# Kernel tuning notes

Measured on AMD Instinct MI355X. Metric: run time of the kernel, lower is better.

## Reference

```python
import jax, jax.numpy as jnp
import numpy as np

HIDDEN = 768
NUM_BLOCKS = 8
BLOCK = HIDDEN // NUM_BLOCKS
LAMBDA = 0.01
SCALE = 0.02


def softshrink(v, lam):
    return jnp.sign(v) * jnp.maximum(jnp.abs(v) - lam, 0.0)


def setup_inputs() -> dict:
    key = jax.random.key(0)
    ks = jax.random.split(key, 5)
    B, S = 4, 8192
    x = jax.random.normal(ks[0], (B, S, HIDDEN), dtype=jnp.float32)
    w1 = SCALE * jax.random.normal(ks[1], (2, NUM_BLOCKS, BLOCK, BLOCK), dtype=jnp.float32)
    b1 = SCALE * jax.random.normal(ks[2], (2, NUM_BLOCKS, BLOCK), dtype=jnp.float32)
    w2 = SCALE * jax.random.normal(ks[3], (2, NUM_BLOCKS, BLOCK, BLOCK), dtype=jnp.float32)
    b2 = SCALE * jax.random.normal(ks[4], (2, NUM_BLOCKS, BLOCK), dtype=jnp.float32)
    return {"x": x, "w1": w1, "b1": b1, "w2": w2, "b2": b2}


def reference(x, w1, b1, w2, b2):
    bias = x
    dtype = x.dtype
    xf = x.astype(jnp.float32)
    B, S, C = xf.shape
    M = S // 2 + 1  # total modes; hard_thresholding_fraction=1.0 -> all kept
    X = jnp.fft.rfft(xf, axis=1, norm="ortho")  # [B, M, C] complex64
    X = X.reshape(B, M, NUM_BLOCKS, BLOCK)
    xr, xi = X.real, X.imag
    # layer 1: complex block-diagonal matmul + relu
    mul = lambda inp, w: jnp.einsum("bmnd,ndk->bmnk", inp, w)
    o1r = jax.nn.relu(mul(xr, w1[0]) - mul(xi, w1[1]) + b1[0])
    o1i = jax.nn.relu(mul(xi, w1[0]) + mul(xr, w1[1]) + b1[1])
    # layer 2
    o2r = mul(o1r, w2[0]) - mul(o1i, w2[1]) + b2[0]
    o2i = mul(o1r, w2[1]) + mul(o1i, w2[0]) + b2[1]
    # softshrink applied elementwise to real and imag parts
    o2r = softshrink(o2r, LAMBDA)
    o2i = softshrink(o2i, LAMBDA)
    Y = (o2r + 1j * o2i).reshape(B, M, C)
    y = jnp.fft.irfft(Y, n=S, axis=1, norm="ortho").astype(dtype)
    return y + bias
```

## Files before the change

kernel.cpp:

```cpp
#include <hip/hip_runtime.h>
#include <hip/hip_bf16.h>

#define HIDDEN 768
#define NB 8
#define BLK 96
#define S_LEN 8192
#define H_LEN 4096
#define M_LEN 4097
#define MP 4160
#define BATCH 4
#define KBIG 192
#define TMOD 64
#define APITCH 100

#define TWO_PI 6.28318530717958647692f
#define INV_SQRT_N 0.011048543456039806f
#define C_INV 0.022097086912079612f
#define LAM 0.01f

typedef __attribute__((ext_vector_type(8))) short short8;
typedef __attribute__((ext_vector_type(4))) float float4v;

__device__ __forceinline__ short f2bf(float f) {
    __hip_bfloat16 h = __float2bfloat16(f);
    return *reinterpret_cast<short*>(&h);
}
__device__ __forceinline__ float bf2f(unsigned short s) {
    __hip_bfloat16 h = *reinterpret_cast<__hip_bfloat16*>(&s);
    return __bfloat162float(h);
}
__device__ __forceinline__ unsigned pack2bf(float a, float b) {
    return (unsigned)(unsigned short)f2bf(a) | ((unsigned)(unsigned short)f2bf(b) << 16);
}
__device__ __forceinline__ float2 cmul(float2 a, float2 b) {
    return make_float2(a.x * b.x - a.y * b.y, a.x * b.y + a.y * b.x);
}

__global__ __launch_bounds__(256) void prep_weights(const float* __restrict__ w1,
                                                    const float* __restrict__ w2,
                                                    const float* __restrict__ b1,
                                                    const float* __restrict__ b2,
                                                    short* __restrict__ WT1,
                                                    short* __restrict__ WT2,
                                                    float* __restrict__ bb1,
                                                    float* __restrict__ bb2) {
    int idx = blockIdx.x * 256 + threadIdx.x;
    if (idx < NB * KBIG * KBIG) {
        int n = idx / (KBIG * KBIG);
        int r = idx % (KBIG * KBIG);
        int op = r / KBIG;
        int kin = r % KBIG;
        int oc = op >> 1;
        int oim = op & 1;
        int d = kin >> 1;
        int im = kin & 1;
        {
            float w0 = w1[((size_t)(0 * NB + n) * BLK + d) * BLK + oc];
            float wi = w1[((size_t)(1 * NB + n) * BLK + d) * BLK + oc];
            float v = oim ? (im ? w0 : wi) : (im ? -wi : w0);
            WT1[idx] = f2bf(v);
        }
        {
            float w0 = w2[((size_t)(0 * NB + n) * BLK + d) * BLK + oc];
            float wi = w2[((size_t)(1 * NB + n) * BLK + d) * BLK + oc];
            float v = oim ? (im ? w0 : wi) : (im ? -wi : w0);
            WT2[idx] = f2bf(v);
        }
    }
    if (idx < NB * KBIG) {
        int n = idx / KBIG, op = idx % KBIG;
        int oc = op >> 1, oim = op & 1;
        bb1[idx] = oim ? b1[(1 * NB + n) * BLK + oc] : b1[(0 * NB + n) * BLK + oc];
        bb2[idx] = oim ? b2[(1 * NB + n) * BLK + oc] : b2[(0 * NB + n) * BLK + oc];
    }
}

__global__ __launch_bounds__(256) void init_twiddles(float2* __restrict__ tw4k,
                                                     float2* __restrict__ tw8k) {
    int i = blockIdx.x * 256 + threadIdx.x;
    if (i < 4096) {
        float ang = -TWO_PI * (float)i * (1.0f / 4096.0f);
        tw4k[i] = make_float2(cosf(ang), sinf(ang));
    }
    if (i <= 4096) {
        float ang = -TWO_PI * (float)i * (1.0f / 8192.0f);
        tw8k[i] = make_float2(cosf(ang), sinf(ang));
    }
}

__global__ __launch_bounds__(256) void transpose_in(const float* __restrict__ x,
                                                    __hip_bfloat16* __restrict__ xT) {
    __shared__ float t[32][33];
    const int cb = blockIdx.x, sb = blockIdx.y, b = blockIdx.z;
    const int tx = threadIdx.x & 31, ty = threadIdx.x >> 5;
    const float* xp = x + ((size_t)b * S_LEN + sb * 32) * HIDDEN + cb * 32;
    for (int i = 0; i < 4; i++)
        t[ty + 8 * i][tx] = xp[(size_t)(ty + 8 * i) * HIDDEN + tx];
    __syncthreads();
    __hip_bfloat16* xq = xT + ((size_t)b * HIDDEN + cb * 32) * S_LEN + sb * 32;
    for (int i = 0; i < 4; i++)
        xq[(size_t)(ty + 8 * i) * S_LEN + tx] = __float2bfloat16(t[tx][ty + 8 * i]);
}

template<bool INV>
__device__ __forceinline__ void dft16(float2* v) {
    const float s3 = INV ? -1.f : 1.f;
    constexpr float C1 = 0.92387953251128674f;
    constexpr float S1 = 0.38268343236508977f;
    constexpr float R2 = 0.70710678118654752f;
    float2 a[16];
    #pragma unroll
    for (int na = 0; na < 4; na++) {
        float2 x0 = v[na], x1 = v[na + 4], x2 = v[na + 8], x3 = v[na + 12];
        float t0x = x0.x + x2.x, t0y = x0.y + x2.y;
        float t1x = x0.x - x2.x, t1y = x0.y - x2.y;
        float t2x = x1.x + x3.x, t2y = x1.y + x3.y;
        float t3x = x1.x - x3.x, t3y = x1.y - x3.y;
        a[na]      = make_float2(t0x + t2x, t0y + t2y);
        a[na + 8]  = make_float2(t0x - t2x, t0y - t2y);
        a[na + 4]  = make_float2(t1x + s3 * t3y, t1y - s3 * t3x);
        a[na + 12] = make_float2(t1x - s3 * t3y, t1y + s3 * t3x);
    }
    auto tw = [s3](float2 z, float ce, float se) {
        return make_float2(z.x * ce + s3 * z.y * se, z.y * ce - s3 * z.x * se);
    };
    a[5]  = tw(a[5],  C1,  S1);
    a[6]  = tw(a[6],  R2,  R2);
    a[7]  = tw(a[7],  S1,  C1);
    a[9]  = tw(a[9],  R2,  R2);
    a[10] = tw(a[10], 0.f, 1.f);
    a[11] = tw(a[11], -R2, R2);
    a[13] = tw(a[13], S1,  C1);
    a[14] = tw(a[14], -R2, R2);
    a[15] = tw(a[15], -C1, -S1);
    #pragma unroll
    for (int kb = 0; kb < 4; kb++) {
        float2 x0 = a[4 * kb], x1 = a[4 * kb + 1], x2 = a[4 * kb + 2], x3 = a[4 * kb + 3];
        float t0x = x0.x + x2.x, t0y = x0.y + x2.y;
        float t1x = x0.x - x2.x, t1y = x0.y - x2.y;
        float t2x = x1.x + x3.x, t2y = x1.y + x3.y;
        float t3x = x1.x - x3.x, t3y = x1.y - x3.y;
        v[kb]      = make_float2(t0x + t2x, t0y + t2y);
        v[kb + 8]  = make_float2(t0x - t2x, t0y - t2y);
        v[kb + 4]  = make_float2(t1x + s3 * t3y, t1y - s3 * t3x);
        v[kb + 12] = make_float2(t1x - s3 * t3y, t1y + s3 * t3x);
    }
}

template<bool INV>
__device__ __forceinline__ void fft3pass(float2* v, float2* arr,
                                         const float2* __restrict__ tw4k, int t) {
    const float sg = INV ? -1.f : 1.f;
    const int n0 = t & 15;
    const int hi = t >> 4;

    dft16<INV>(v);
    arr[n0 * 17 + hi] = v[0];
    #pragma unroll
    for (int p = 1; p < 16; p++) {
        float2 w = tw4k[(t * p) & 4095];
        arr[(n0 + 16 * p) * 17 + hi] = cmul(v[p], make_float2(w.x, sg * w.y));
    }
    __syncthreads();

    #pragma unroll
    for (int n1 = 0; n1 < 16; n1++) v[n1] = arr[t * 17 + n1];
    __syncthreads();
    dft16<INV>(v);
    arr[hi * 17 + n0] = v[0];
    #pragma unroll
    for (int q = 1; q < 16; q++) {
        float2 w = tw4k[(16 * n0 * q) & 4095];
        arr[(hi + 16 * q) * 17 + n0] = cmul(v[q], make_float2(w.x, sg * w.y));
    }
    __syncthreads();

    #pragma unroll
    for (int i = 0; i < 16; i++) v[i] = arr[t * 17 + i];
    dft16<INV>(v);
}

__global__ __launch_bounds__(256, 4) void fft_fwd(const __hip_bfloat16* __restrict__ xT,
                                                  unsigned int* __restrict__ Xc,
                                                  const float2* __restrict__ tw4k,
                                                  const float2* __restrict__ tw8k) {
    __shared__ __align__(16) float2 arr[256 * 17];
    const int wg = blockIdx.x;
    const int t = threadIdx.x;
    const __hip_bfloat162* xrow = (const __hip_bfloat162*)(xT + (size_t)wg * S_LEN);

    float2 v[16];
    #pragma unroll
    for (int j = 0; j < 16; j++) {
        __hip_bfloat162 pz = xrow[t + 256 * j];
        v[j] = make_float2(__bfloat162float(pz.x), __bfloat162float(pz.y));
    }

    fft3pass<false>(v, arr, tw4k, t);

    __syncthreads();
    #pragma unroll
    for (int k0 = 0; k0 < 16; k0++) arr[t + 256 * k0] = v[k0];
    __syncthreads();

    unsigned int* Xrow = Xc + (size_t)wg * MP;
    for (int m = t; m <= H_LEN; m += 256) {
        int ia = m & (H_LEN - 1);
        int ib = (H_LEN - m) & (H_LEN - 1);
        float2 za = arr[ia];
        float2 zb = arr[ib];
        float er = 0.5f * (za.x + zb.x), ei = 0.5f * (za.y - zb.y);
        float dr = za.x - zb.x, di = za.y + zb.y;
        float or_ = 0.5f * di, oi = -0.5f * dr;
        float2 tt = tw8k[m];
        float xrv = (er + tt.x * or_ - tt.y * oi) * INV_SQRT_N;
        float xiv = (ei + tt.x * oi + tt.y * or_) * INV_SQRT_N;
        unsigned wd = (unsigned short)f2bf(xrv) | ((unsigned)(unsigned short)f2bf(xiv) << 16);
        Xrow[m] = wd;
    }
}

__global__ __launch_bounds__(256, 3) void mlp_mfma(const short* __restrict__ WT1,
                                                   const short* __restrict__ WT2,
                                                   const float* __restrict__ bb1,
                                                   const float* __restrict__ bb2,
                                                   unsigned int* __restrict__ Xc) {
    __shared__ __align__(16) unsigned int actA[TMOD * APITCH];
    __shared__ __align__(16) unsigned int actB[TMOD * APITCH];
    const int tid = threadIdx.x;
    const int chunk = blockIdx.x;
    const int n = blockIdx.y;
    const int b = blockIdx.z;
    const int m0 = chunk * TMOD;
    unsigned int* __restrict__ Xrow0 =
        Xc + ((size_t)b * HIDDEN + (size_t)n * BLK) * MP + m0;

    const int w = tid >> 6;
    const int l15 = tid & 15;
    const int q = (tid >> 4) & 3;
    const int outw = w * 48;
    const int mstg = tid & 63;

    #pragma unroll
    for (int dp = 0; dp < 6; dp++) {
        int d0 = dp * 16 + w * 4;
        uint4 vv;
        vv.x = Xrow0[(size_t)(d0 + 0) * MP + mstg];
        vv.y = Xrow0[(size_t)(d0 + 1) * MP + mstg];
        vv.z = Xrow0[(size_t)(d0 + 2) * MP + mstg];
        vv.w = Xrow0[(size_t)(d0 + 3) * MP + mstg];
        *(uint4*)&actA[mstg * APITCH + d0] = vv;
    }

    short8 wf[3][6];
    for (int nl = 0; nl < 3; nl++)
        for (int ks = 0; ks < 6; ks++)
            wf[nl][ks] = *(const short8*)(WT1 + ((size_t)n * KBIG + outw + nl * 16 + l15) * KBIG + ks * 32 + q * 8);

    __syncthreads();

    for (int mt = 0; mt < 4; mt++) {
        float4v acc[3];
        for (int nl = 0; nl < 3; nl++)
            acc[nl] = *(const float4v*)(bb1 + n * KBIG + outw + nl * 16 + q * 4);
        #pragma unroll
        for (int ks = 0; ks < 6; ks++) {
            short8 bf = *(const short8*)(&actA[(mt * 16 + l15) * APITCH + ks * 16 + q * 4]);
            acc[0] = __builtin_amdgcn_mfma_f32_16x16x32_bf16(wf[0][ks], bf, acc[0], 0, 0, 0);
            acc[1] = __builtin_amdgcn_mfma_f32_16x16x32_bf16(wf[1][ks], bf, acc[1], 0, 0, 0);
            acc[2] = __builtin_amdgcn_mfma_f32_16x16x32_bf16(wf[2][ks], bf, acc[2], 0, 0, 0);
        }
        #pragma unroll
        for (int nl = 0; nl < 3; nl++) {
            uint2 st;
            st.x = pack2bf(fmaxf(acc[nl][0], 0.f), fmaxf(acc[nl][1], 0.f));
            st.y = pack2bf(fmaxf(acc[nl][2], 0.f), fmaxf(acc[nl][3], 0.f));
            *(uint2*)&actB[(mt * 16 + l15) * APITCH + outw / 2 + nl * 8 + q * 2] = st;
        }
    }

    short8 wf2[3][6];
    for (int nl = 0; nl < 3; nl++)
        for (int ks = 0; ks < 6; ks++)
            wf2[nl][ks] = *(const short8*)(WT2 + ((size_t)n * KBIG + outw + nl * 16 + l15) * KBIG + ks * 32 + q * 8);

    __syncthreads();

    for (int mt = 0; mt < 4; mt++) {
        float4v acc[3];
        for (int nl = 0; nl < 3; nl++)
            acc[nl] = *(const float4v*)(bb2 + n * KBIG + outw + nl * 16 + q * 4);
        #pragma unroll
        for (int ks = 0; ks < 6; ks++) {
            short8 bf = *(const short8*)(&actB[(mt * 16 + l15) * APITCH + ks * 16 + q * 4]);
            acc[0] = __builtin_amdgcn_mfma_f32_16x16x32_bf16(wf2[0][ks], bf, acc[0], 0, 0, 0);
            acc[1] = __builtin_amdgcn_mfma_f32_16x16x32_bf16(wf2[1][ks], bf, acc[1], 0, 0, 0);
            acc[2] = __builtin_amdgcn_mfma_f32_16x16x32_bf16(wf2[2][ks], bf, acc[2], 0, 0, 0);
        }
        #pragma unroll
        for (int nl = 0; nl < 3; nl++) {
            float v0 = acc[nl][0], v1 = acc[nl][1], v2 = acc[nl][2], v3 = acc[nl][3];
            v0 = copysignf(fmaxf(fabsf(v0) - LAM, 0.f), v0);
            v1 = copysignf(fmaxf(fabsf(v1) - LAM, 0.f), v1);
            v2 = copysignf(fmaxf(fabsf(v2) - LAM, 0.f), v2);
            v3 = copysignf(fmaxf(fabsf(v3) - LAM, 0.f), v3);
            uint2 st;
            st.x = pack2bf(v0, v1);
            st.y = pack2bf(v2, v3);
            *(uint2*)&actA[(mt * 16 + l15) * APITCH + outw / 2 + nl * 8 + q * 2] = st;
        }
    }
    __syncthreads();

    #pragma unroll
    for (int dp = 0; dp < 6; dp++) {
        int d0 = dp * 16 + w * 4;
        uint4 vv = *(const uint4*)&actA[mstg * APITCH + d0];
        Xrow0[(size_t)(d0 + 0) * MP + mstg] = vv.x;
        Xrow0[(size_t)(d0 + 1) * MP + mstg] = vv.y;
        Xrow0[(size_t)(d0 + 2) * MP + mstg] = vv.z;
        Xrow0[(size_t)(d0 + 3) * MP + mstg] = vv.w;
    }
}

__global__ __launch_bounds__(256, 4) void fft_inv(const unsigned int* __restrict__ Xc,
                                                  __hip_bfloat16* __restrict__ yT,
                                                  const float2* __restrict__ tw4k,
                                                  const float2* __restrict__ tw8k) {
    __shared__ __align__(16) float2 arr[256 * 17];
    const int wg = blockIdx.x;
    const int t = threadIdx.x;
    const unsigned int* Xrow = Xc + (size_t)wg * MP;

    float2 v[16];
    #pragma unroll
    for (int j = 0; j < 16; j++) {
        int m = t + 256 * j;
        unsigned va = Xrow[m];
        unsigned vb = Xrow[H_LEN - m];
        float arv = bf2f((unsigned short)(va & 0xFFFF));
        float aiv = bf2f((unsigned short)(va >> 16));
        float brv = bf2f((unsigned short)(vb & 0xFFFF));
        float biv = bf2f((unsigned short)(vb >> 16));
        if (m == 0) { aiv = 0.f; biv = 0.f; }
        float er = 0.5f * (arv + brv), ei = 0.5f * (aiv - biv);
        float dr = arv - brv, di = aiv + biv;
        float2 tt = tw8k[m];
        float wcs = tt.x, wsn = -tt.y;
        float or_ = 0.5f * (wcs * dr - wsn * di);
        float oi = 0.5f * (wcs * di + wsn * dr);
        v[j] = make_float2(er - oi, ei + or_);
    }

    fft3pass<true>(v, arr, tw4k, t);

    __hip_bfloat162* orow = (__hip_bfloat162*)(yT + (size_t)wg * S_LEN);
    #pragma unroll
    for (int k0 = 0; k0 < 16; k0++) {
        __hip_bfloat162 w;
        w.x = __float2bfloat16(C_INV * v[k0].x);
        w.y = __float2bfloat16(C_INV * v[k0].y);
        orow[t + 256 * k0] = w;
    }
}

__global__ __launch_bounds__(256) void add_out(const __hip_bfloat16* __restrict__ yT,
                                               const float* __restrict__ x,
                                               float* __restrict__ out) {
    __shared__ float t[32][33];
    const int cb = blockIdx.x, sb = blockIdx.y, b = blockIdx.z;
    const int tx = threadIdx.x & 31, ty = threadIdx.x >> 5;
    const __hip_bfloat16* yp = yT + ((size_t)b * HIDDEN + cb * 32) * S_LEN + sb * 32;
    for (int i = 0; i < 4; i++)
        t[ty + 8 * i][tx] = __bfloat162float(yp[(size_t)(ty + 8 * i) * S_LEN + tx]);
    __syncthreads();
    const size_t off = ((size_t)b * S_LEN + sb * 32) * HIDDEN + cb * 32;
    const float* xp = x + off;
    float* op = out + off;
    for (int i = 0; i < 4; i++)
        op[(size_t)(ty + 8 * i) * HIDDEN + tx] =
            xp[(size_t)(ty + 8 * i) * HIDDEN + tx] + t[tx][ty + 8 * i];
}

extern "C" void kernel_launch(void* const* d_in, const int* in_sizes, int n_in,
                              void* d_out, int out_size, void* d_ws, size_t ws_size,
                              hipStream_t stream) {
    const float* x  = (const float*)d_in[0];
    const float* w1 = (const float*)d_in[1];
    const float* b1 = (const float*)d_in[2];
    const float* w2 = (const float*)d_in[3];
    const float* b2 = (const float*)d_in[4];
    float* out = (float*)d_out;

    char* p = (char*)d_ws;
    __hip_bfloat16* xT = (__hip_bfloat16*)p;           p += (size_t)BATCH * HIDDEN * S_LEN * 2;
    unsigned int*   Xc = (unsigned int*)p;             p += (size_t)BATCH * HIDDEN * MP * 4;
    short* WT1 = (short*)p;                            p += (size_t)NB * KBIG * KBIG * 2;
    short* WT2 = (short*)p;                            p += (size_t)NB * KBIG * KBIG * 2;
    float* bb1 = (float*)p;                            p += (size_t)NB * KBIG * 4;
    float* bb2 = (float*)p;                            p += (size_t)NB * KBIG * 4;
    float2* tw4k = (float2*)p;                         p += (size_t)4096 * sizeof(float2);
    float2* tw8k = (float2*)p;                         p += (size_t)4100 * sizeof(float2);

    prep_weights<<<(NB * KBIG * KBIG + 255) / 256, 256, 0, stream>>>(
        w1, w2, b1, b2, WT1, WT2, bb1, bb2);

    init_twiddles<<<17, 256, 0, stream>>>(tw4k, tw8k);

    transpose_in<<<dim3(HIDDEN / 32, S_LEN / 32, BATCH), 256, 0, stream>>>(x, xT);

    fft_fwd<<<BATCH * HIDDEN, 256, 0, stream>>>(xT, Xc, tw4k, tw8k);

    mlp_mfma<<<dim3(65, NB, BATCH), 256, 0, stream>>>(WT1, WT2, bb1, bb2, Xc);

    fft_inv<<<BATCH * HIDDEN, 256, 0, stream>>>(Xc, xT , tw4k, tw8k);

    add_out<<<dim3(HIDDEN / 32, S_LEN / 32, BATCH), 256, 0, stream>>>(xT, x, out);
}
```

Baseline: 387.7 us.

## Vectorize transposes with 64x64 tiles and halve MLP mode tile size

The input and output transposes now use 64x64 tiles, with float4 and short4 global accesses in place of scalar ones, to cut global memory transactions. The MLP kernel processes 32 modes per block instead of 64, which doubles the grid (129 chunks) for better occupancy and load balance. In exchange, each MLP block reloads its weight fragments for half as much work, and the larger LDS tiles in the transposes may reduce occupancy there.

```diff
diff --git a/kernel.cpp b/kernel.cpp
--- a/kernel.cpp
+++ b/kernel.cpp
@@ -10,7 +10,7 @@
 #define MP 4160
 #define BATCH 4
 #define KBIG 192
-#define TMOD 64
+#define TMOD 32
 #define APITCH 100
 
 #define TWO_PI 6.28318530717958647692f
@@ -90,16 +90,35 @@
 
 __global__ __launch_bounds__(256) void transpose_in(const float* __restrict__ x,
                                                     __hip_bfloat16* __restrict__ xT) {
-    __shared__ float t[32][33];
+    __shared__ float t[64][66];
     const int cb = blockIdx.x, sb = blockIdx.y, b = blockIdx.z;
-    const int tx = threadIdx.x & 31, ty = threadIdx.x >> 5;
-    const float* xp = x + ((size_t)b * S_LEN + sb * 32) * HIDDEN + cb * 32;
-    for (int i = 0; i < 4; i++)
-        t[ty + 8 * i][tx] = xp[(size_t)(ty + 8 * i) * HIDDEN + tx];
-    __syncthreads();
-    __hip_bfloat16* xq = xT + ((size_t)b * HIDDEN + cb * 32) * S_LEN + sb * 32;
-    for (int i = 0; i < 4; i++)
-        xq[(size_t)(ty + 8 * i) * S_LEN + tx] = __float2bfloat16(t[tx][ty + 8 * i]);
+    const int tid = threadIdx.x;
+    {
+        const int cq = tid & 15, sr = tid >> 4;
+        const float* xp = x + ((size_t)(b * S_LEN + sb * 64 + sr)) * HIDDEN + cb * 64 + cq * 4;
+        #pragma unroll
+        for (int i = 0; i < 4; i++) {
+            float4 v = *(const float4*)(xp + (size_t)16 * i * HIDDEN);
+            int s = sr + 16 * i;
+            t[cq * 4 + 0][s] = v.x;
+            t[cq * 4 + 1][s] = v.y;
+            t[cq * 4 + 2][s] = v.z;
+            t[cq * 4 + 3][s] = v.w;
+        }
+    }
+    __syncthreads();
+    {
+        const int s4 = tid & 15, cr = tid >> 4;
+        #pragma unroll
+        for (int i = 0; i < 4; i++) {
+            int c = cr + 16 * i;
+            float2 a = *(const float2*)&t[c][s4 * 4];
+            float2 bv = *(const float2*)&t[c][s4 * 4 + 2];
+            short4 o;
+            o.x = f2bf(a.x); o.y = f2bf(a.y); o.z = f2bf(bv.x); o.w = f2bf(bv.y);
+            *(short4*)(xT + ((size_t)(b * HIDDEN + cb * 64 + c)) * S_LEN + sb * 64 + s4 * 4) = o;
+        }
+    }
 }
 
 template<bool INV>
@@ -239,11 +258,12 @@
     const int l15 = tid & 15;
     const int q = (tid >> 4) & 3;
     const int outw = w * 48;
-    const int mstg = tid & 63;
-
-    #pragma unroll
-    for (int dp = 0; dp < 6; dp++) {
-        int d0 = dp * 16 + w * 4;
+    const int mstg = tid & 31;
+    const int g8 = tid >> 5;
+
+    #pragma unroll
+    for (int dp = 0; dp < 3; dp++) {
+        int d0 = g8 * 12 + dp * 4;
         uint4 vv;
         vv.x = Xrow0[(size_t)(d0 + 0) * MP + mstg];
         vv.y = Xrow0[(size_t)(d0 + 1) * MP + mstg];
@@ -259,7 +279,7 @@
 
     __syncthreads();
 
-    for (int mt = 0; mt < 4; mt++) {
+    for (int mt = 0; mt < 2; mt++) {
         float4v acc[3];
         for (int nl = 0; nl < 3; nl++)
             acc[nl] = *(const float4v*)(bb1 + n * KBIG + outw + nl * 16 + q * 4);
@@ -286,7 +306,7 @@
 
     __syncthreads();
 
-    for (int mt = 0; mt < 4; mt++) {
+    for (int mt = 0; mt < 2; mt++) {
         float4v acc[3];
         for (int nl = 0; nl < 3; nl++)
             acc[nl] = *(const float4v*)(bb2 + n * KBIG + outw + nl * 16 + q * 4);
@@ -313,8 +333,8 @@
     __syncthreads();
 
     #pragma unroll
-    for (int dp = 0; dp < 6; dp++) {
-        int d0 = dp * 16 + w * 4;
+    for (int dp = 0; dp < 3; dp++) {
+        int d0 = g8 * 12 + dp * 4;
         uint4 vv = *(const uint4*)&actA[mstg * APITCH + d0];
         Xrow0[(size_t)(d0 + 0) * MP + mstg] = vv.x;
         Xrow0[(size_t)(d0 + 1) * MP + mstg] = vv.y;
@@ -367,19 +387,36 @@
 __global__ __launch_bounds__(256) void add_out(const __hip_bfloat16* __restrict__ yT,
                                                const float* __restrict__ x,
                                                float* __restrict__ out) {
-    __shared__ float t[32][33];
+    __shared__ float t[64][66];
     const int cb = blockIdx.x, sb = blockIdx.y, b = blockIdx.z;
-    const int tx = threadIdx.x & 31, ty = threadIdx.x >> 5;
-    const __hip_bfloat16* yp = yT + ((size_t)b * HIDDEN + cb * 32) * S_LEN + sb * 32;
-    for (int i = 0; i < 4; i++)
-        t[ty + 8 * i][tx] = __bfloat162float(yp[(size_t)(ty + 8 * i) * S_LEN + tx]);
-    __syncthreads();
-    const size_t off = ((size_t)b * S_LEN + sb * 32) * HIDDEN + cb * 32;
-    const float* xp = x + off;
-    float* op = out + off;
-    for (int i = 0; i < 4; i++)
-        op[(size_t)(ty + 8 * i) * HIDDEN + tx] =
-            xp[(size_t)(ty + 8 * i) * HIDDEN + tx] + t[tx][ty + 8 * i];
+    const int tid = threadIdx.x;
+    {
+        const int s4 = tid & 15, cr = tid >> 4;
+        #pragma unroll
+        for (int i = 0; i < 4; i++) {
+            int c = cr + 16 * i;
+            short4 v = *(const short4*)(yT + ((size_t)(b * HIDDEN + cb * 64 + c)) * S_LEN + sb * 64 + s4 * 4);
+            t[s4 * 4 + 0][c] = bf2f((unsigned short)v.x);
+            t[s4 * 4 + 1][c] = bf2f((unsigned short)v.y);
+            t[s4 * 4 + 2][c] = bf2f((unsigned short)v.z);
+            t[s4 * 4 + 3][c] = bf2f((unsigned short)v.w);
+        }
+    }
+    __syncthreads();
+    {
+        const int cq = tid & 15, sr = tid >> 4;
+        #pragma unroll
+        for (int i = 0; i < 4; i++) {
+            int s = sr + 16 * i;
+            const size_t off = ((size_t)(b * S_LEN + sb * 64 + s)) * HIDDEN + cb * 64 + cq * 4;
+            float4 xv = *(const float4*)(x + off);
+            float2 a = *(const float2*)&t[s][cq * 4];
+            float2 bv = *(const float2*)&t[s][cq * 4 + 2];
+            float4 ov;
+            ov.x = xv.x + a.x; ov.y = xv.y + a.y; ov.z = xv.z + bv.x; ov.w = xv.w + bv.y;
+            *(float4*)(out + off) = ov;
+        }
+    }
 }
 
 extern "C" void kernel_launch(void* const* d_in, const int* in_sizes, int n_in,
@@ -407,13 +444,13 @@
 
     init_twiddles<<<17, 256, 0, stream>>>(tw4k, tw8k);
 
-    transpose_in<<<dim3(HIDDEN / 32, S_LEN / 32, BATCH), 256, 0, stream>>>(x, xT);
+    transpose_in<<<dim3(HIDDEN / 64, S_LEN / 64, BATCH), 256, 0, stream>>>(x, xT);
 
     fft_fwd<<<BATCH * HIDDEN, 256, 0, stream>>>(xT, Xc, tw4k, tw8k);
 
-    mlp_mfma<<<dim3(65, NB, BATCH), 256, 0, stream>>>(WT1, WT2, bb1, bb2, Xc);
+    mlp_mfma<<<dim3(129, NB, BATCH), 256, 0, stream>>>(WT1, WT2, bb1, bb2, Xc);
 
     fft_inv<<<BATCH * HIDDEN, 256, 0, stream>>>(Xc, xT , tw4k, tw8k);
 
-    add_out<<<dim3(HIDDEN / 32, S_LEN / 32, BATCH), 256, 0, stream>>>(xT, x, out);
-}
+    add_out<<<dim3(HIDDEN / 64, S_LEN / 64, BATCH), 256, 0, stream>>>(xT, x, out);
+}
```

Measured after the change: 405.2 us. 4.5% more time.
